# Performance work log

Measured on AMD Instinct MI355X. Metric: run time of the kernel, lower is better.

Reference implementation:

```python
import jax, jax.numpy as jnp
import numpy as np

H = 1024; NH = 16; HD = H // NH  # hidden, heads, head_dim

def setup_inputs() -> dict:
    key = jax.random.key(0)
    ks = jax.random.split(key, 9)
    s = 1.0 / np.sqrt(H)
    return {
        "hidden_states": jax.random.normal(ks[0], (2, 2048, H), jnp.float32),
        "Wq": jax.random.uniform(ks[1], (H, H), jnp.float32, -s, s),
        "bq": jnp.zeros((H,), jnp.float32),
        "Wk": jax.random.uniform(ks[2], (H, H), jnp.float32, -s, s),
        "bk": jnp.zeros((H,), jnp.float32),
        "Wv": jax.random.uniform(ks[3], (H, H), jnp.float32, -s, s),
        "bv": jnp.zeros((H,), jnp.float32),
        "Wo": jax.random.uniform(ks[4], (H, H), jnp.float32, -s, s),
        "bo": jnp.zeros((H,), jnp.float32),
    }

def reference(hidden_states, Wq, bq, Wk, bk, Wv, bv, Wo, bo):
    B, S, _ = hidden_states.shape
    def heads(x):  # [B,S,H] -> [B,NH,S,HD]
        return x.reshape(B, S, NH, HD).transpose(0, 2, 1, 3)
    q = heads(hidden_states @ Wq + bq)
    k = heads(hidden_states @ Wk + bk)
    v = heads(hidden_states @ Wv + bv)
    scores = jnp.einsum('bhqd,bhkd->bhqk', q, k) / jnp.sqrt(jnp.float32(HD))
    causal = jnp.where(jnp.tril(jnp.ones((S, S), bool)), 0.0, -jnp.inf)
    probs = jax.nn.softmax(scores + causal[None, None], axis=-1)
    ctx = jnp.einsum('bhqk,bhkd->bhqd', probs, v)
    ctx = ctx.transpose(0, 2, 1, 3).reshape(B, S, H)
    return ctx @ Wo + bo
```

## Files before the change

### kernel.cpp

```cpp
#include <hip/hip_runtime.h>
#include <hip/hip_bf16.h>

#define BB 2
#define SS 2048
#define HH 1024
#define NHH 16
#define HDD 64
#define MM (BB*SS)
#define QKV_N (3*HH)

typedef _Float16 f16x8 __attribute__((ext_vector_type(8)));
typedef _Float16 f16x4 __attribute__((ext_vector_type(4)));
typedef float f32x4 __attribute__((ext_vector_type(4)));

#define MFMA16(a,b,c)  __builtin_amdgcn_mfma_f32_16x16x32_f16((a),(b),(c),0,0,0)
#define MFMA16K16(a,b,c) __builtin_amdgcn_mfma_f32_16x16x16f16((a),(b),(c),0,0,0)

__device__ __forceinline__ void gl2lds16(const _Float16* g, _Float16* l) {
    __builtin_amdgcn_global_load_lds(
        (const __attribute__((address_space(1))) void*)g,
        (__attribute__((address_space(3))) void*)l, 16, 0, 0);
}

__device__ __forceinline__ float fexp2(float x) { return __builtin_amdgcn_exp2f(x); }

__global__ __launch_bounds__(256) void prep_kernel(
    const float* __restrict__ X,
    const float* __restrict__ W0, const float* __restrict__ W1,
    const float* __restrict__ W2, const float* __restrict__ W3,
    _Float16* __restrict__ Xh,
    _Float16* __restrict__ WqkvT, _Float16* __restrict__ WoT)
{
    __shared__ float t[64][65];
    int z = blockIdx.z;
    int tid = threadIdx.x;
    if (z == 4) {
        int base = (blockIdx.y * 16 + blockIdx.x) * 256 + tid;
        const float4* xin = (const float4*)X;
        f16x4* xout = (f16x4*)Xh;
#pragma unroll
        for (int i = 0; i < 16; ++i) {
            float4 v = xin[base + i * 65536];
            f16x4 hh = {(_Float16)v.x, (_Float16)v.y, (_Float16)v.z, (_Float16)v.w};
            xout[base + i * 65536] = hh;
        }
        return;
    }
    const float* src = (z == 0) ? W0 : (z == 1) ? W1 : (z == 2) ? W2 : W3;
    _Float16* dst = (z < 3) ? (WqkvT + (size_t)z * HH * HH) : WoT;
    int k0 = blockIdx.y * 64, n0 = blockIdx.x * 64;
#pragma unroll
    for (int p = 0; p < 4; ++p) {
        int row = p * 16 + (tid >> 4);
        int col4 = (tid & 15) * 4;
        float4 v = *(const float4*)&src[(size_t)(k0 + row) * HH + n0 + col4];
        t[row][col4 + 0] = v.x; t[row][col4 + 1] = v.y;
        t[row][col4 + 2] = v.z; t[row][col4 + 3] = v.w;
    }
    __syncthreads();
#pragma unroll
    for (int p = 0; p < 2; ++p) {
        int nc = p * 32 + (tid >> 3);
        int ch = tid & 7;
        f16x8 o;
#pragma unroll
        for (int j = 0; j < 8; ++j) o[j] = (_Float16)t[ch * 8 + j][nc];
        *(f16x8*)&dst[(size_t)(n0 + nc) * HH + k0 + ch * 8] = o;
    }
}

__global__ __launch_bounds__(256) void gemm128_kernel(
    const _Float16* __restrict__ A, const _Float16* __restrict__ Bt,
    const float* __restrict__ bias0, const float* __restrict__ bias1, const float* __restrict__ bias2,
    _Float16* __restrict__ Qh, _Float16* __restrict__ Kh, _Float16* __restrict__ Vt)
{
    const int K = HH;
    const int NT = K / 32;
    __shared__ _Float16 smem[24576];

    int row0 = blockIdx.y * 128, n0 = blockIdx.x * 128;
    int tid = threadIdx.x;
    int w = tid >> 6, l = tid & 63, m16 = l & 15, quad = l >> 4;
    int wm = w >> 1, wn = w & 1;

    int srow = w * 32 + (l >> 2);
    int sch = (l & 3) ^ ((l >> 2) & 3) ^ ((l >> 4) & 3);
    const _Float16* aptr = A + (size_t)(row0 + srow) * K + sch * 8;
    const _Float16* bptr = Bt + (size_t)(n0 + srow) * K + sch * 8;

    int gsw = (m16 & 3) ^ ((m16 >> 2) & 3);
    int acol = (quad ^ gsw) * 8;

    f32x4 zero4 = {0.f, 0.f, 0.f, 0.f};
    f32x4 acc[4][4];
#pragma unroll
    for (int i = 0; i < 4; ++i)
#pragma unroll
        for (int j = 0; j < 4; ++j) acc[i][j] = zero4;

    auto stage = [&](int t, int s) {
        int k0 = t * 32;
        int ao = s * 4096 + (w * 32) * 32;
        int bo = 12288 + s * 4096 + (w * 32) * 32;
        gl2lds16(aptr + k0, smem + ao);
        gl2lds16(aptr + (size_t)16 * K + k0, smem + ao + 16 * 32);
        gl2lds16(bptr + k0, smem + bo);
        gl2lds16(bptr + (size_t)16 * K + k0, smem + bo + 16 * 32);
    };

    stage(0, 0);
    stage(1, 1);
    int cur = 0;
    for (int t = 0; t < NT; ++t) {
        if (t < NT - 1) asm volatile("s_waitcnt vmcnt(4)" ::: "memory");
        else            asm volatile("s_waitcnt vmcnt(0)" ::: "memory");
        asm volatile("s_barrier" ::: "memory");
        if (t + 2 < NT) {
            int nxt = cur + 2; if (nxt >= 3) nxt -= 3;
            stage(t + 2, nxt);
        }
        const _Float16* Asr = smem + cur * 4096;
        const _Float16* Bsr = smem + 12288 + cur * 4096;
        f16x8 af[4], bf[4];
#pragma unroll
        for (int i = 0; i < 4; ++i)
            af[i] = *(const f16x8*)&Asr[(wm * 64 + i * 16 + m16) * 32 + acol];
#pragma unroll
        for (int j = 0; j < 4; ++j)
            bf[j] = *(const f16x8*)&Bsr[(wn * 64 + j * 16 + m16) * 32 + acol];
#pragma unroll
        for (int i = 0; i < 4; ++i)
#pragma unroll
            for (int j = 0; j < 4; ++j)
                acc[i][j] = MFMA16(af[i], bf[j], acc[i][j]);
        cur = (cur == 2) ? 0 : cur + 1;
    }

    int which = n0 >> 10;
    const float* bias = (which == 0) ? bias0 : (which == 1) ? bias1 : bias2;
    __syncthreads();
#pragma unroll
    for (int j = 0; j < 4; ++j) {
        int n_local = wn * 64 + j * 16 + m16;
        float bi = bias[(n0 + n_local) & 1023];
#pragma unroll
        for (int i = 0; i < 4; ++i)
#pragma unroll
            for (int r = 0; r < 4; ++r) {
                int m_local = wm * 64 + i * 16 + quad * 4 + r;
                float v = acc[i][j][r] + bi;
                if (which == 0) v *= 0.18033688011112042f;
                if (which == 2) smem[n_local * 132 + m_local] = (_Float16)v;
                else            smem[m_local * 132 + n_local] = (_Float16)v;
            }
    }
    __syncthreads();

    int b = row0 >> 11, s0 = row0 & 2047;
    if (which == 2) {
#pragma unroll
        for (int p = 0; p < 8; ++p) {
            int n_local = p * 16 + (tid >> 4);
            int schunk = tid & 15;
            f16x8 v = *(const f16x8*)&smem[n_local * 132 + schunk * 8];
            int nw = (n0 + n_local) & 1023;
            int hh = nw >> 6, d = nw & 63;
            *(f16x8*)&Vt[((size_t)(b * NHH + hh) * HDD + d) * SS + s0 + schunk * 8] = v;
        }
    } else {
        _Float16* dst = (which == 0) ? Qh : Kh;
        int hh0 = (n0 & 1023) >> 6;
#pragma unroll
        for (int p = 0; p < 8; ++p) {
            int m_local = p * 16 + (tid >> 4);
            int seg = tid & 15;
            f16x8 v = *(const f16x8*)&smem[m_local * 132 + seg * 8];
            int hh = hh0 + (seg >> 3), d = (seg & 7) * 8;
            *(f16x8*)&dst[((size_t)(b * NHH + hh) * SS + s0 + m_local) * HDD + d] = v;
        }
    }
}

__global__ __launch_bounds__(256) void gemm_op_kernel(
    const _Float16* __restrict__ A, const _Float16* __restrict__ Bt,
    const float* __restrict__ bias0, float* __restrict__ Out)
{
    const int K = HH;
    const int NT = K / 32;
    __shared__ _Float16 smem[18432];

    int row0 = blockIdx.y * 128, n0 = blockIdx.x * 64;
    int tid = threadIdx.x;
    int w = tid >> 6, l = tid & 63, m16 = l & 15, quad = l >> 4;

    int sch = (l & 3) ^ ((l >> 2) & 3) ^ ((l >> 4) & 3);
    const _Float16* aptr = A + (size_t)(row0 + w * 32 + (l >> 2)) * K + sch * 8;
    const _Float16* bptr = Bt + (size_t)(n0 + w * 16 + (l >> 2)) * K + sch * 8;

    int gsw = (m16 & 3) ^ ((m16 >> 2) & 3);
    int acol = (quad ^ gsw) * 8;

    f32x4 zero4 = {0.f, 0.f, 0.f, 0.f};
    f32x4 acc[2][4];
#pragma unroll
    for (int i = 0; i < 2; ++i)
#pragma unroll
        for (int j = 0; j < 4; ++j) acc[i][j] = zero4;

    auto stage = [&](int t, int s) {
        int k0 = t * 32;
        int ao = s * 4096 + (w * 32) * 32;
        int bo = 12288 + s * 2048 + (w * 16) * 32;
        gl2lds16(aptr + k0, smem + ao);
        gl2lds16(aptr + (size_t)16 * K + k0, smem + ao + 16 * 32);
        gl2lds16(bptr + k0, smem + bo);
    };

    stage(0, 0);
    stage(1, 1);
    int cur = 0;
    for (int t = 0; t < NT; ++t) {
        if (t < NT - 1) asm volatile("s_waitcnt vmcnt(3)" ::: "memory");
        else            asm volatile("s_waitcnt vmcnt(0)" ::: "memory");
        asm volatile("s_barrier" ::: "memory");
        if (t + 2 < NT) {
            int nxt = cur + 2; if (nxt >= 3) nxt -= 3;
            stage(t + 2, nxt);
        }
        const _Float16* Asr = smem + cur * 4096;
        const _Float16* Bsr = smem + 12288 + cur * 2048;
        f16x8 af[2], bf[4];
#pragma unroll
        for (int i = 0; i < 2; ++i)
            af[i] = *(const f16x8*)&Asr[(w * 32 + i * 16 + m16) * 32 + acol];
#pragma unroll
        for (int j = 0; j < 4; ++j)
            bf[j] = *(const f16x8*)&Bsr[(j * 16 + m16) * 32 + acol];
#pragma unroll
        for (int i = 0; i < 2; ++i)
#pragma unroll
            for (int j = 0; j < 4; ++j)
                acc[i][j] = MFMA16(af[i], bf[j], acc[i][j]);
        cur = (cur == 2) ? 0 : cur + 1;
    }

#pragma unroll
    for (int j = 0; j < 4; ++j) {
        int n = n0 + j * 16 + m16;
        float bi = bias0[n];
#pragma unroll
        for (int i = 0; i < 2; ++i)
#pragma unroll
            for (int r = 0; r < 4; ++r) {
                int mg = row0 + w * 32 + i * 16 + quad * 4 + r;
                Out[(size_t)mg * HH + n] = acc[i][j][r] + bi;
            }
    }
}

__global__ __launch_bounds__(512, 4) void attn_kernel(
    const _Float16* __restrict__ Qh, const _Float16* __restrict__ Kh,
    const _Float16* __restrict__ Vt, _Float16* __restrict__ Ctx)
{
    __shared__ _Float16 KV[3 * 8192];

    int tid = threadIdx.x;
    int w = tid >> 6, l = tid & 63;
    int m16 = l & 15, quad = l >> 4;
    int b = blockIdx.z, h = blockIdx.y;
    int tA = blockIdx.x, tB = 31 - tA;
    int half = w >> 2, wq = w & 3;
    int myT = half ? tB : tA;

    const _Float16* Q = Qh + (size_t)(b * NHH + h) * SS * HDD;
    const _Float16* K = Kh + (size_t)(b * NHH + h) * SS * HDD;
    const _Float16* V = Vt + (size_t)(b * NHH + h) * HDD * SS;

    int q = myT * 64 + wq * 16 + m16;
    f16x8 aq0 = *(const f16x8*)(Q + (size_t)q * HDD + quad * 8);
    f16x8 aq1 = *(const f16x8*)(Q + (size_t)q * HDD + 32 + quad * 8);

    int srow = w * 8 + (l >> 3);
    int sch = (l & 7) ^ (l >> 3);
    const _Float16* kg = K + (size_t)srow * HDD + sch * 8;
    const _Float16* vg = V + (size_t)srow * SS + sch * 8;

    auto stage = [&](int t, int s) {
        int kt = t * 64;
        _Float16* kb = &KV[s * 8192];
        _Float16* vb = &KV[s * 8192 + 4096];
        gl2lds16(kg + (size_t)kt * HDD, kb + (w * 8) * 64);
        gl2lds16(vg + kt, vb + (w * 8) * 64);
    };

    int swz = m16 & 7;
    int cka = (quad ^ swz) * 8;
    int ckb = ((quad + 4) ^ swz) * 8;
    int vco[4];
#pragma unroll
    for (int s = 0; s < 4; ++s)
        vco[s] = (((s * 2 + (quad >> 1)) ^ swz) * 8) + (quad & 1) * 4;

    f32x4 zero4 = {0.f, 0.f, 0.f, 0.f};
    const f16x4 ones4 = {(_Float16)1.f, (_Float16)1.f, (_Float16)1.f, (_Float16)1.f};
    f32x4 o[4];
#pragma unroll
    for (int c = 0; c < 4; ++c) o[c] = zero4;
    f32x4 lacc = zero4;

    stage(0, 0);
    stage(1, 1);
    int cur = 0;
    for (int t = 0; t <= tB; ++t) {
        int kt = t * 64;
        if (t < tB) asm volatile("s_waitcnt vmcnt(2)" ::: "memory");
        else        asm volatile("s_waitcnt vmcnt(0)" ::: "memory");
        asm volatile("s_barrier" ::: "memory");
        if (t + 2 <= tB) {
            int nxt = cur + 2; if (nxt >= 3) nxt -= 3;
            stage(t + 2, nxt);
        }

        if (t <= myT) {
            const _Float16* kb = &KV[cur * 8192];
            const _Float16* vb = &KV[cur * 8192 + 4096];
            f16x8 bk[4][2];
#pragma unroll
            for (int s = 0; s < 4; ++s) {
                const _Float16* kr = kb + (s * 16 + m16) * 64;
                bk[s][0] = *(const f16x8*)(kr + cka);
                bk[s][1] = *(const f16x8*)(kr + ckb);
            }
            f16x4 av[4][4];
#pragma unroll
            for (int c = 0; c < 4; ++c) {
                const _Float16* vr = vb + (c * 16 + m16) * 64;
#pragma unroll
                for (int s = 0; s < 4; ++s)
                    av[c][s] = *(const f16x4*)(vr + vco[s]);
            }

            f32x4 st[4];
#pragma unroll
            for (int s = 0; s < 4; ++s) {
                st[s] = MFMA16(bk[s][0], aq0, zero4);
                st[s] = MFMA16(bk[s][1], aq1, st[s]);
            }
            f16x4 pt[4];
            if (t == myT) {
#pragma unroll
                for (int s = 0; s < 4; ++s)
#pragma unroll
                    for (int r = 0; r < 4; ++r) {
                        float p = fexp2(st[s][r]);
                        int key = kt + s * 16 + quad * 4 + r;
                        if (key > q) p = 0.f;
                        pt[s][r] = (_Float16)p;
                    }
            } else {
#pragma unroll
                for (int s = 0; s < 4; ++s)
#pragma unroll
                    for (int r = 0; r < 4; ++r)
                        pt[s][r] = (_Float16)fexp2(st[s][r]);
            }
#pragma unroll
            for (int s = 0; s < 4; ++s)
                lacc = MFMA16K16(ones4, pt[s], lacc);
#pragma unroll
            for (int c = 0; c < 4; ++c)
#pragma unroll
                for (int s = 0; s < 4; ++s)
                    o[c] = MFMA16K16(av[c][s], pt[s], o[c]);
        }

        cur = (cur == 2) ? 0 : cur + 1;
    }

    float inv = 1.0f / lacc[0];
    size_t rowoff = ((size_t)(b * SS) + q) * HH + h * HDD;
#pragma unroll
    for (int c = 0; c < 4; ++c) {
        f16x4 ov;
#pragma unroll
        for (int r = 0; r < 4; ++r) ov[r] = (_Float16)(o[c][r] * inv);
        *(f16x4*)&Ctx[rowoff + c * 16 + quad * 4] = ov;
    }
}

extern "C" void kernel_launch(void* const* d_in, const int* in_sizes, int n_in,
                              void* d_out, int out_size, void* d_ws, size_t ws_size,
                              hipStream_t stream) {
    const float* hs = (const float*)d_in[0];
    const float* Wq = (const float*)d_in[1];
    const float* bq = (const float*)d_in[2];
    const float* Wk = (const float*)d_in[3];
    const float* bk = (const float*)d_in[4];
    const float* Wv = (const float*)d_in[5];
    const float* bv = (const float*)d_in[6];
    const float* Wo = (const float*)d_in[7];
    const float* bo = (const float*)d_in[8];
    float* out = (float*)d_out;

    size_t off = 0;
    auto alloc = [&](size_t bytes) {
        void* p = (char*)d_ws + off;
        off += (bytes + 255) & ~(size_t)255;
        return p;
    };
    _Float16* Xh    = (_Float16*)alloc((size_t)MM * HH * 2);
    _Float16* WqkvT = (_Float16*)alloc((size_t)3 * HH * HH * 2);
    _Float16* WoT   = (_Float16*)alloc((size_t)HH * HH * 2);
    _Float16* Qh    = (_Float16*)alloc((size_t)BB * NHH * SS * HDD * 2);
    _Float16* Kh    = (_Float16*)alloc((size_t)BB * NHH * SS * HDD * 2);
    _Float16* Vt    = (_Float16*)alloc((size_t)BB * NHH * SS * HDD * 2);
    _Float16* Ctx   = (_Float16*)alloc((size_t)MM * HH * 2);

    prep_kernel<<<dim3(16, 16, 5), 256, 0, stream>>>(
        hs, Wq, Wk, Wv, Wo, Xh, WqkvT, WoT);
    gemm128_kernel<<<dim3(QKV_N / 128, MM / 128), 256, 0, stream>>>(
        Xh, WqkvT, bq, bk, bv, Qh, Kh, Vt);
    attn_kernel<<<dim3(16, NHH, BB), 512, 0, stream>>>(Qh, Kh, Vt, Ctx);
    gemm_op_kernel<<<dim3(HH / 64, MM / 128), 256, 0, stream>>>(
        Ctx, WoT, bo, out);
}
```

Baseline: 185.2 us.

## Shrink QKV GEMM LDS to double buffer and use 128x128 tiles for output GEMM

The QKV projection GEMM drops from a triple-buffered 48KB LDS layout to a double-buffered 32KB one with a two-barrier prefetch loop. It requests 5 blocks per CU and splits the epilogue into two 64-row halves so the staging buffer fits the smaller LDS. The output projection GEMM now reuses the old 128x128 triple-buffered kernel instead of 128x64 tiles, which halves its grid and raises per-block reuse. The aim is more resident blocks for the QKV GEMM and fewer, more efficient blocks for the output GEMM. The cost is less prefetch depth, an extra barrier per K step, and fewer blocks to fill the CUs in the output GEMM.

```diff
diff --git a/kernel.cpp b/kernel.cpp
--- a/kernel.cpp
+++ b/kernel.cpp
@@ -69,10 +69,127 @@
     }
 }
 
-__global__ __launch_bounds__(256) void gemm128_kernel(
+__global__ __launch_bounds__(256, 5) void gemm_qkv_kernel(
     const _Float16* __restrict__ A, const _Float16* __restrict__ Bt,
     const float* __restrict__ bias0, const float* __restrict__ bias1, const float* __restrict__ bias2,
     _Float16* __restrict__ Qh, _Float16* __restrict__ Kh, _Float16* __restrict__ Vt)
+{
+    const int K = HH;
+    const int NT = K / 32;
+    __shared__ _Float16 smem[16384];
+
+    int row0 = blockIdx.y * 128, n0 = blockIdx.x * 128;
+    int tid = threadIdx.x;
+    int w = tid >> 6, l = tid & 63, m16 = l & 15, quad = l >> 4;
+    int wm = w >> 1, wn = w & 1;
+
+    int srow = w * 32 + (l >> 2);
+    int sch = (l & 3) ^ ((l >> 2) & 3) ^ ((l >> 4) & 3);
+    const _Float16* aptr = A + (size_t)(row0 + srow) * K + sch * 8;
+    const _Float16* bptr = Bt + (size_t)(n0 + srow) * K + sch * 8;
+
+    int gsw = (m16 & 3) ^ ((m16 >> 2) & 3);
+    int acol = (quad ^ gsw) * 8;
+
+    f32x4 zero4 = {0.f, 0.f, 0.f, 0.f};
+    f32x4 acc[4][4];
+#pragma unroll
+    for (int i = 0; i < 4; ++i)
+#pragma unroll
+        for (int j = 0; j < 4; ++j) acc[i][j] = zero4;
+
+    auto stage = [&](int t) {
+        int s = (t & 1) * 4096;
+        int k0 = t * 32;
+        int ao = s + (w * 32) * 32;
+        int bo = 8192 + s + (w * 32) * 32;
+        gl2lds16(aptr + k0, smem + ao);
+        gl2lds16(aptr + (size_t)16 * K + k0, smem + ao + 16 * 32);
+        gl2lds16(bptr + k0, smem + bo);
+        gl2lds16(bptr + (size_t)16 * K + k0, smem + bo + 16 * 32);
+    };
+
+    stage(0);
+    for (int t = 0; t < NT; ++t) {
+        asm volatile("s_barrier" ::: "memory");
+        if (t + 1 < NT) {
+            stage(t + 1);
+            asm volatile("s_waitcnt vmcnt(4)" ::: "memory");
+        } else {
+            asm volatile("s_waitcnt vmcnt(0)" ::: "memory");
+        }
+        asm volatile("s_barrier" ::: "memory");
+
+        const _Float16* Asr = smem + (t & 1) * 4096;
+        const _Float16* Bsr = smem + 8192 + (t & 1) * 4096;
+        f16x8 af[4], bf[4];
+#pragma unroll
+        for (int i = 0; i < 4; ++i)
+            af[i] = *(const f16x8*)&Asr[(wm * 64 + i * 16 + m16) * 32 + acol];
+#pragma unroll
+        for (int j = 0; j < 4; ++j)
+            bf[j] = *(const f16x8*)&Bsr[(wn * 64 + j * 16 + m16) * 32 + acol];
+#pragma unroll
+        for (int i = 0; i < 4; ++i)
+#pragma unroll
+            for (int j = 0; j < 4; ++j)
+                acc[i][j] = MFMA16(af[i], bf[j], acc[i][j]);
+    }
+
+    int which = n0 >> 10;
+    const float* bias = (which == 0) ? bias0 : (which == 1) ? bias1 : bias2;
+    int b = row0 >> 11, s0 = row0 & 2047;
+
+#pragma unroll
+    for (int rh = 0; rh < 2; ++rh) {
+        __syncthreads();
+        if (wm == rh) {
+#pragma unroll
+            for (int j = 0; j < 4; ++j) {
+                int n_local = wn * 64 + j * 16 + m16;
+                float bi = bias[(n0 + n_local) & 1023];
+#pragma unroll
+                for (int i = 0; i < 4; ++i)
+#pragma unroll
+                    for (int r = 0; r < 4; ++r) {
+                        int m_loc = i * 16 + quad * 4 + r;
+                        float v = acc[i][j][r] + bi;
+                        if (which == 0) v *= 0.18033688011112042f;
+                        if (which == 2) smem[n_local * 68 + m_loc] = (_Float16)v;
+                        else            smem[m_loc * 132 + n_local] = (_Float16)v;
+                    }
+            }
+        }
+        __syncthreads();
+        int hs0 = s0 + rh * 64;
+        if (which == 2) {
+#pragma unroll
+            for (int p = 0; p < 4; ++p) {
+                int n_local = p * 32 + (tid >> 3);
+                int schunk = tid & 7;
+                f16x8 v = *(const f16x8*)&smem[n_local * 68 + schunk * 8];
+                int nw = (n0 + n_local) & 1023;
+                int hh = nw >> 6, d = nw & 63;
+                *(f16x8*)&Vt[((size_t)(b * NHH + hh) * HDD + d) * SS + hs0 + schunk * 8] = v;
+            }
+        } else {
+            _Float16* dst = (which == 0) ? Qh : Kh;
+            int hh0 = (n0 & 1023) >> 6;
+#pragma unroll
+            for (int p = 0; p < 4; ++p) {
+                int m_local = p * 16 + (tid >> 4);
+                int seg = tid & 15;
+                f16x8 v = *(const f16x8*)&smem[m_local * 132 + seg * 8];
+                int hh = hh0 + (seg >> 3), d = (seg & 7) * 8;
+                *(f16x8*)&dst[((size_t)(b * NHH + hh) * SS + hs0 + m_local) * HDD + d] = v;
+            }
+        }
+    }
+}
+
+__global__ __launch_bounds__(256) void gemm_out_kernel(
+    const _Float16* __restrict__ A, const _Float16* __restrict__ Bt,
+    const float* __restrict__ bias0, float* __restrict__ Out)
 {
     const int K = HH;
     const int NT = K / 32;
@@ -136,123 +253,15 @@
         cur = (cur == 2) ? 0 : cur + 1;
     }
 
-    int which = n0 >> 10;
-    const float* bias = (which == 0) ? bias0 : (which == 1) ? bias1 : bias2;
-    __syncthreads();
 #pragma unroll
     for (int j = 0; j < 4; ++j) {
-        int n_local = wn * 64 + j * 16 + m16;
-        float bi = bias[(n0 + n_local) & 1023];
+        int n = n0 + wn * 64 + j * 16 + m16;
+        float bi = bias0[n];
 #pragma unroll
         for (int i = 0; i < 4; ++i)
 #pragma unroll
             for (int r = 0; r < 4; ++r) {
-                int m_local = wm * 64 + i * 16 + quad * 4 + r;
-                float v = acc[i][j][r] + bi;
-                if (which == 0) v *= 0.18033688011112042f;
-                if (which == 2) smem[n_local * 132 + m_local] = (_Float16)v;
-                else            smem[m_local * 132 + n_local] = (_Float16)v;
-            }
-    }
-    __syncthreads();
-
-    int b = row0 >> 11, s0 = row0 & 2047;
-    if (which == 2) {
-#pragma unroll
-        for (int p = 0; p < 8; ++p) {
-            int n_local = p * 16 + (tid >> 4);
-            int schunk = tid & 15;
-            f16x8 v = *(const f16x8*)&smem[n_local * 132 + schunk * 8];
-            int nw = (n0 + n_local) & 1023;
-            int hh = nw >> 6, d = nw & 63;
-            *(f16x8*)&Vt[((size_t)(b * NHH + hh) * HDD + d) * SS + s0 + schunk * 8] = v;
-        }
-    } else {
-        _Float16* dst = (which == 0) ? Qh : Kh;
-        int hh0 = (n0 & 1023) >> 6;
-#pragma unroll
-        for (int p = 0; p < 8; ++p) {
-            int m_local = p * 16 + (tid >> 4);
-            int seg = tid & 15;
-            f16x8 v = *(const f16x8*)&smem[m_local * 132 + seg * 8];
-            int hh = hh0 + (seg >> 3), d = (seg & 7) * 8;
-            *(f16x8*)&dst[((size_t)(b * NHH + hh) * SS + s0 + m_local) * HDD + d] = v;
-        }
-    }
-}
-
-__global__ __launch_bounds__(256) void gemm_op_kernel(
-    const _Float16* __restrict__ A, const _Float16* __restrict__ Bt,
-    const float* __restrict__ bias0, float* __restrict__ Out)
-{
-    const int K = HH;
-    const int NT = K / 32;
-    __shared__ _Float16 smem[18432];
-
-    int row0 = blockIdx.y * 128, n0 = blockIdx.x * 64;
-    int tid = threadIdx.x;
-    int w = tid >> 6, l = tid & 63, m16 = l & 15, quad = l >> 4;
-
-    int sch = (l & 3) ^ ((l >> 2) & 3) ^ ((l >> 4) & 3);
-    const _Float16* aptr = A + (size_t)(row0 + w * 32 + (l >> 2)) * K + sch * 8;
-    const _Float16* bptr = Bt + (size_t)(n0 + w * 16 + (l >> 2)) * K + sch * 8;
-
-    int gsw = (m16 & 3) ^ ((m16 >> 2) & 3);
-    int acol = (quad ^ gsw) * 8;
-
-    f32x4 zero4 = {0.f, 0.f, 0.f, 0.f};
-    f32x4 acc[2][4];
-#pragma unroll
-    for (int i = 0; i < 2; ++i)
-#pragma unroll
-        for (int j = 0; j < 4; ++j) acc[i][j] = zero4;
-
-    auto stage = [&](int t, int s) {
-        int k0 = t * 32;
-        int ao = s * 4096 + (w * 32) * 32;
-        int bo = 12288 + s * 2048 + (w * 16) * 32;
-        gl2lds16(aptr + k0, smem + ao);
-        gl2lds16(aptr + (size_t)16 * K + k0, smem + ao + 16 * 32);
-        gl2lds16(bptr + k0, smem + bo);
-    };
-
-    stage(0, 0);
-    stage(1, 1);
-    int cur = 0;
-    for (int t = 0; t < NT; ++t) {
-        if (t < NT - 1) asm volatile("s_waitcnt vmcnt(3)" ::: "memory");
-        else            asm volatile("s_waitcnt vmcnt(0)" ::: "memory");
-        asm volatile("s_barrier" ::: "memory");
-        if (t + 2 < NT) {
-            int nxt = cur + 2; if (nxt >= 3) nxt -= 3;
-            stage(t + 2, nxt);
-        }
-        const _Float16* Asr = smem + cur * 4096;
-        const _Float16* Bsr = smem + 12288 + cur * 2048;
-        f16x8 af[2], bf[4];
-#pragma unroll
-        for (int i = 0; i < 2; ++i)
-            af[i] = *(const f16x8*)&Asr[(w * 32 + i * 16 + m16) * 32 + acol];
-#pragma unroll
-        for (int j = 0; j < 4; ++j)
-            bf[j] = *(const f16x8*)&Bsr[(j * 16 + m16) * 32 + acol];
-#pragma unroll
-        for (int i = 0; i < 2; ++i)
-#pragma unroll
-            for (int j = 0; j < 4; ++j)
-                acc[i][j] = MFMA16(af[i], bf[j], acc[i][j]);
-        cur = (cur == 2) ? 0 : cur + 1;
-    }
-
-#pragma unroll
-    for (int j = 0; j < 4; ++j) {
-        int n = n0 + j * 16 + m16;
-        float bi = bias0[n];
-#pragma unroll
-        for (int i = 0; i < 2; ++i)
-#pragma unroll
-            for (int r = 0; r < 4; ++r) {
-                int mg = row0 + w * 32 + i * 16 + quad * 4 + r;
+                int mg = row0 + wm * 64 + i * 16 + quad * 4 + r;
                 Out[(size_t)mg * HH + n] = acc[i][j][r] + bi;
             }
     }
@@ -418,9 +427,9 @@
 
     prep_kernel<<<dim3(16, 16, 5), 256, 0, stream>>>(
         hs, Wq, Wk, Wv, Wo, Xh, WqkvT, WoT);
-    gemm128_kernel<<<dim3(QKV_N / 128, MM / 128), 256, 0, stream>>>(
+    gemm_qkv_kernel<<<dim3(QKV_N / 128, MM / 128), 256, 0, stream>>>(
         Xh, WqkvT, bq, bk, bv, Qh, Kh, Vt);
     attn_kernel<<<dim3(16, NHH, BB), 512, 0, stream>>>(Qh, Kh, Vt, Ctx);
-    gemm_op_kernel<<<dim3(HH / 64, MM / 128), 256, 0, stream>>>(
+    gemm_out_kernel<<<dim3(HH / 128, MM / 128), 256, 0, stream>>>(
         Ctx, WoT, bo, out);
 }
```

After: 181.3 us. -2.1%, faster.

## Rewrite output projection GEMM as 128x128 tile with split-K across two warp groups

Applied to the files above, without the earlier changes.

The output projection GEMM moves from 128x64 tiles with 4 warps to 128x128 tiles with 8 warps. The warps form two groups that each handle half of K, and the partial sums are combined through shared memory before the bias is added and the result stored. The goal is more operand reuse per tile and more warps per block to hide latency. In exchange it uses 96KB of LDS, launches half as many blocks (256), and adds a shared-memory reduction step. The QKV kernel is only renamed.

```diff
diff --git a/kernel.cpp b/kernel.cpp
--- a/kernel.cpp
+++ b/kernel.cpp
@@ -69,7 +69,7 @@
     }
 }
 
-__global__ __launch_bounds__(256) void gemm128_kernel(
+__global__ __launch_bounds__(256) void gemm_qkv_kernel(
     const _Float16* __restrict__ A, const _Float16* __restrict__ Bt,
     const float* __restrict__ bias0, const float* __restrict__ bias1, const float* __restrict__ bias2,
     _Float16* __restrict__ Qh, _Float16* __restrict__ Kh, _Float16* __restrict__ Vt)
@@ -181,80 +181,102 @@
     }
 }
 
-__global__ __launch_bounds__(256) void gemm_op_kernel(
+__global__ __launch_bounds__(512, 2) void gemm_out_kernel(
     const _Float16* __restrict__ A, const _Float16* __restrict__ Bt,
     const float* __restrict__ bias0, float* __restrict__ Out)
 {
     const int K = HH;
-    const int NT = K / 32;
-    __shared__ _Float16 smem[18432];
-
-    int row0 = blockIdx.y * 128, n0 = blockIdx.x * 64;
+    const int NT = 16;
+    __shared__ _Float16 smem[49152];
+
+    int row0 = blockIdx.y * 128, n0 = blockIdx.x * 128;
     int tid = threadIdx.x;
     int w = tid >> 6, l = tid & 63, m16 = l & 15, quad = l >> 4;
-
+    int kg = w >> 2, wl = w & 3;
+    int wm = wl >> 1, wn = wl & 1;
+    int kbase = kg * 512;
+    _Float16* gsm = smem + kg * 24576;
+
+    int srow = wl * 32 + (l >> 2);
     int sch = (l & 3) ^ ((l >> 2) & 3) ^ ((l >> 4) & 3);
-    const _Float16* aptr = A + (size_t)(row0 + w * 32 + (l >> 2)) * K + sch * 8;
-    const _Float16* bptr = Bt + (size_t)(n0 + w * 16 + (l >> 2)) * K + sch * 8;
+    const _Float16* aptr = A + (size_t)(row0 + srow) * K + kbase + sch * 8;
+    const _Float16* bptr = Bt + (size_t)(n0 + srow) * K + kbase + sch * 8;
 
     int gsw = (m16 & 3) ^ ((m16 >> 2) & 3);
     int acol = (quad ^ gsw) * 8;
 
     f32x4 zero4 = {0.f, 0.f, 0.f, 0.f};
-    f32x4 acc[2][4];
-#pragma unroll
-    for (int i = 0; i < 2; ++i)
+    f32x4 acc[4][4];
+#pragma unroll
+    for (int i = 0; i < 4; ++i)
 #pragma unroll
         for (int j = 0; j < 4; ++j) acc[i][j] = zero4;
 
     auto stage = [&](int t, int s) {
         int k0 = t * 32;
-        int ao = s * 4096 + (w * 32) * 32;
-        int bo = 12288 + s * 2048 + (w * 16) * 32;
-        gl2lds16(aptr + k0, smem + ao);
-        gl2lds16(aptr + (size_t)16 * K + k0, smem + ao + 16 * 32);
-        gl2lds16(bptr + k0, smem + bo);
+        int ao = s * 4096 + (wl * 32) * 32;
+        int bo = 12288 + s * 4096 + (wl * 32) * 32;
+        gl2lds16(aptr + k0, gsm + ao);
+        gl2lds16(aptr + (size_t)16 * K + k0, gsm + ao + 16 * 32);
+        gl2lds16(bptr + k0, gsm + bo);
+        gl2lds16(bptr + (size_t)16 * K + k0, gsm + bo + 16 * 32);
     };
 
     stage(0, 0);
     stage(1, 1);
     int cur = 0;
     for (int t = 0; t < NT; ++t) {
-        if (t < NT - 1) asm volatile("s_waitcnt vmcnt(3)" ::: "memory");
+        if (t < NT - 1) asm volatile("s_waitcnt vmcnt(4)" ::: "memory");
         else            asm volatile("s_waitcnt vmcnt(0)" ::: "memory");
         asm volatile("s_barrier" ::: "memory");
         if (t + 2 < NT) {
             int nxt = cur + 2; if (nxt >= 3) nxt -= 3;
             stage(t + 2, nxt);
         }
-        const _Float16* Asr = smem + cur * 4096;
-        const _Float16* Bsr = smem + 12288 + cur * 2048;
-        f16x8 af[2], bf[4];
-#pragma unroll
-        for (int i = 0; i < 2; ++i)
-            af[i] = *(const f16x8*)&Asr[(w * 32 + i * 16 + m16) * 32 + acol];
+        const _Float16* Asr = gsm + cur * 4096;
+        const _Float16* Bsr = gsm + 12288 + cur * 4096;
+        f16x8 af[4], bf[4];
+#pragma unroll
+        for (int i = 0; i < 4; ++i)
+            af[i] = *(const f16x8*)&Asr[(wm * 64 + i * 16 + m16) * 32 + acol];
 #pragma unroll
         for (int j = 0; j < 4; ++j)
-            bf[j] = *(const f16x8*)&Bsr[(j * 16 + m16) * 32 + acol];
-#pragma unroll
-        for (int i = 0; i < 2; ++i)
+            bf[j] = *(const f16x8*)&Bsr[(wn * 64 + j * 16 + m16) * 32 + acol];
+#pragma unroll
+        for (int i = 0; i < 4; ++i)
 #pragma unroll
             for (int j = 0; j < 4; ++j)
                 acc[i][j] = MFMA16(af[i], bf[j], acc[i][j]);
         cur = (cur == 2) ? 0 : cur + 1;
     }
 
-#pragma unroll
-    for (int j = 0; j < 4; ++j) {
-        int n = n0 + j * 16 + m16;
-        float bi = bias0[n];
-#pragma unroll
-        for (int i = 0; i < 2; ++i)
-#pragma unroll
-            for (int r = 0; r < 4; ++r) {
-                int mg = row0 + w * 32 + i * 16 + quad * 4 + r;
-                Out[(size_t)mg * HH + n] = acc[i][j][r] + bi;
-            }
+    float* red = (float*)smem;
+    __syncthreads();
+    if (kg == 1) {
+        float* slot = red + (size_t)(wl * 64 + l) * 65;
+#pragma unroll
+        for (int i = 0; i < 4; ++i)
+#pragma unroll
+            for (int j = 0; j < 4; ++j)
+#pragma unroll
+                for (int r = 0; r < 4; ++r)
+                    slot[i * 16 + j * 4 + r] = acc[i][j][r];
+    }
+    __syncthreads();
+    if (kg == 0) {
+        const float* slot = red + (size_t)(wl * 64 + l) * 65;
+#pragma unroll
+        for (int j = 0; j < 4; ++j) {
+            int n = n0 + wn * 64 + j * 16 + m16;
+            float bi = bias0[n];
+#pragma unroll
+            for (int i = 0; i < 4; ++i)
+#pragma unroll
+                for (int r = 0; r < 4; ++r) {
+                    int mg = row0 + wm * 64 + i * 16 + quad * 4 + r;
+                    Out[(size_t)mg * HH + n] = acc[i][j][r] + slot[i * 16 + j * 4 + r] + bi;
+                }
+        }
     }
 }
 
@@ -418,9 +440,9 @@
 
     prep_kernel<<<dim3(16, 16, 5), 256, 0, stream>>>(
         hs, Wq, Wk, Wv, Wo, Xh, WqkvT, WoT);
-    gemm128_kernel<<<dim3(QKV_N / 128, MM / 128), 256, 0, stream>>>(
+    gemm_qkv_kernel<<<dim3(QKV_N / 128, MM / 128), 256, 0, stream>>>(
         Xh, WqkvT, bq, bk, bv, Qh, Kh, Vt);
     attn_kernel<<<dim3(16, NHH, BB), 512, 0, stream>>>(Qh, Kh, Vt, Ctx);
-    gemm_op_kernel<<<dim3(HH / 64, MM / 128), 256, 0, stream>>>(
+    gemm_out_kernel<<<dim3(HH / 128, MM / 128), 512, 0, stream>>>(
         Ctx, WoT, bo, out);
 }
```

After: 178.1 us. 3.9% less time.
